# Kernel optimization log

Measured on AMD Instinct MI355X. Metric: run time of the kernel, lower is better.

## Reference

```python
import jax, jax.numpy as jnp
import numpy as np

SEQ, D, H, FF = 2048, 1024, 16, 4096
HD = D // H  # head_dim = 64


def setup_inputs() -> dict:
    key = jax.random.key(0)
    ks = jax.random.split(key, 13)
    s = lambda k, shape, fan_in: jax.random.normal(k, shape, jnp.float32) / np.sqrt(fan_in)
    return {
        "x":  jax.random.normal(ks[0], (SEQ, D), jnp.float32),
        # per-head Q/K/V linears, batched over the head axis: [H, D, HD]
        "Wq": s(ks[1], (H, D, HD), D), "bq": jnp.zeros((H, HD), jnp.float32),
        "Wk": s(ks[2], (H, D, HD), D), "bk": jnp.zeros((H, HD), jnp.float32),
        "Wv": s(ks[3], (H, D, HD), D), "bv": jnp.zeros((H, HD), jnp.float32),
        "Wp": s(ks[4], (D, D), D),     "bp": jnp.zeros((D,), jnp.float32),
        "W1": s(ks[5], (D, FF), D),    "b1": jnp.zeros((FF,), jnp.float32),
        "W2": s(ks[6], (FF, D), FF),   "b2": jnp.zeros((D,), jnp.float32),
    }


def reference(x, Wq, bq, Wk, bk, Wv, bv, Wp, bp, W1, b1, W2, b2):
    # Batched per-head projections: [H, S, HD]
    Qx = jnp.einsum("sd,hde->hse", x, Wq) + bq[:, None, :]
    Kx = jnp.einsum("sd,hde->hse", x, Wk) + bk[:, None, :]
    Vx = jnp.einsum("sd,hde->hse", x, Wv) + bv[:, None, :]
    # scores[h,s,t] = Qx[h,s]. Kx[h,t] / sqrt(HD); softmax over t (last dim)
    scores = jnp.einsum("hse,hte->hst", Qx, Kx) / jnp.sqrt(jnp.float32(HD))
    attn = jax.nn.softmax(scores, axis=-1)
    # Faithful to source: head[t,e] = sum_s Vx[s,e] * attn[s,t]  (attn^T @ V)
    heads = jnp.einsum("hse,hst->hte", Vx, attn)  # [H, S, HD]
    # concat heads along feature dim (head-major order) -> [S, D]
    concat = jnp.transpose(heads, (1, 0, 2)).reshape(SEQ, H * HD)
    proj = concat @ Wp + bp
    hidden = jax.nn.relu(proj @ W1 + b1)
    out = hidden @ W2 + b2
    return out
```

## Files before the change

kernel.cpp:

```cpp
#include <hip/hip_runtime.h>
#include <math.h>

constexpr int S_  = 2048;
constexpr int D_  = 1024;
constexpr int H_  = 16;
constexpr int HD_ = 64;
constexpr int FF_ = 4096;

typedef short bf16x8 __attribute__((ext_vector_type(8)));
typedef float f32x4  __attribute__((ext_vector_type(4)));

static __device__ __forceinline__ ushort f2bf(float f) {
    union { __bf16 b; ushort u; } c;
    c.b = (__bf16)f;
    return c.u;
}
static __device__ __forceinline__ float bf2f(ushort u) {
    return __uint_as_float(((unsigned)u) << 16);
}

static __device__ __forceinline__ float exp8(float x) {
    return __builtin_amdgcn_exp2f(x * 0.18033688f);
}

static __device__ __forceinline__ void gload_lds16(const void* g, void* l) {
    __builtin_amdgcn_global_load_lds(
        (const __attribute__((address_space(1))) unsigned int*)g,
        (__attribute__((address_space(3))) unsigned int*)l, 16, 0, 0);
}

static __device__ __forceinline__ void tc_tile(
    const float* __restrict__ in, ushort* __restrict__ out,
    int K, int N, int n0, int k0)
{
    __shared__ float Ts[32][33];
    const int tid = threadIdx.x;
    const int r = tid >> 3, c4 = (tid & 7) * 4;
    float4 v = *(const float4*)(in + (size_t)(k0 + r) * N + n0 + c4);
    Ts[r][c4 + 0] = v.x; Ts[r][c4 + 1] = v.y;
    Ts[r][c4 + 2] = v.z; Ts[r][c4 + 3] = v.w;
    __syncthreads();
    ushort4 o;
    o.x = f2bf(Ts[c4 + 0][r]); o.y = f2bf(Ts[c4 + 1][r]);
    o.z = f2bf(Ts[c4 + 2][r]); o.w = f2bf(Ts[c4 + 3][r]);
    *(ushort4*)(out + (size_t)(n0 + r) * K + k0 + c4) = o;
}

__global__ __launch_bounds__(256) void pack_all(
    const float* __restrict__ x,
    const float* __restrict__ Wq, const float* __restrict__ Wk,
    const float* __restrict__ Wv, const float* __restrict__ Wp,
    const float* __restrict__ W1, const float* __restrict__ W2,
    const float* __restrict__ bq, const float* __restrict__ bk,
    const float* __restrict__ bv,
    ushort* __restrict__ xb, ushort* __restrict__ BTqkv,
    ushort* __restrict__ BTp, ushort* __restrict__ BT1,
    ushort* __restrict__ BT2, float* __restrict__ biascat)
{
    const int b = blockIdx.x;
    const int tid = threadIdx.x;
    if (b < 2048) {
        const int i = b * 1024 + tid * 4;
        float4 v = *(const float4*)(x + i);
        ushort4 o;
        o.x = f2bf(v.x); o.y = f2bf(v.y); o.z = f2bf(v.z); o.w = f2bf(v.w);
        *(ushort4*)(xb + i) = o;
    } else if (b < 5120) {
        int j = b - 2048;
        const int which = j >> 10;
        j &= 1023;
        const int hh = j >> 6, t = j & 63;
        const float* W = (which == 0) ? Wq : (which == 1) ? Wk : Wv;
        tc_tile(W + hh * 65536, BTqkv + which * 1024 * 1024 + hh * 65536,
                1024, 64, (t & 1) * 32, (t >> 1) * 32);
    } else if (b < 6144) {
        const int j = b - 5120;
        tc_tile(Wp, BTp, 1024, 1024, (j & 31) * 32, (j >> 5) * 32);
    } else if (b < 10240) {
        const int j = b - 6144;
        tc_tile(W1, BT1, 1024, 4096, (j & 127) * 32, (j >> 7) * 32);
    } else if (b < 14336) {
        const int j = b - 10240;
        tc_tile(W2, BT2, 4096, 1024, (j & 31) * 32, (j >> 5) * 32);
    } else {
        const int i = (b - 14336) * 256 + tid;
        float v = (i < 1024) ? bq[i] : (i < 2048 ? bk[i - 1024] : bv[i - 2048]);
        biascat[i] = v;
    }
}

template <int BM, int BN, int WR, int WC, int KS, int RELU, int OUT>
__global__ __launch_bounds__(WR * WC * 64) void gemm_mfma(
    const ushort* __restrict__ A, const ushort* __restrict__ BT,
    const float* __restrict__ bias, void* __restrict__ Cv,
    void* __restrict__ Cv2, int M, int N, int K)
{
    constexpr int WAVES = WR * WC;
    constexpr int WTM = BM / WR, WTN = BN / WC;
    constexpr int MT = WTM / 16, NT = WTN / 16;
    constexpr int AI = BM / 8;
    constexpr int TI = (BM + BN) / 8;
    constexpr int PW = TI / WAVES;

    __shared__ ushort As[BM * 64];
    __shared__ ushort Bs[BN * 64];

    const int tid = threadIdx.x;
    const int lane = tid & 63;
    const int wave = tid >> 6;
    const int wr = wave / WC, wc = wave % WC;
    const int row16 = lane & 15, kgrp = lane >> 4;
    const int m0 = blockIdx.y * BM, n0 = blockIdx.x * BN;
    const int kOff = (KS > 1) ? blockIdx.z * (K / KS) : 0;

    const int lrow = lane >> 3;
    const int sc8 = (lane & 7) ^ lrow;

    f32x4 acc[MT][NT];
#pragma unroll
    for (int i = 0; i < MT; ++i)
#pragma unroll
        for (int j = 0; j < NT; ++j) acc[i][j] = (f32x4){0.f, 0.f, 0.f, 0.f};

    for (int k0 = kOff; k0 < kOff + K / KS; k0 += 64) {
        __syncthreads();
#pragma unroll
        for (int i = 0; i < PW; ++i) {
            const int inst = wave * PW + i;
            if (inst < AI) {
                const int row = inst * 8;
                gload_lds16(A + (size_t)(m0 + row + lrow) * K + k0 + sc8 * 8,
                            As + row * 64);
            } else {
                const int row = (inst - AI) * 8;
                gload_lds16(BT + (size_t)(n0 + row + lrow) * K + k0 + sc8 * 8,
                            Bs + row * 64);
            }
        }
        __syncthreads();
#pragma unroll
        for (int ks = 0; ks < 2; ++ks) {
            bf16x8 af[MT], bfr[NT];
#pragma unroll
            for (int mt = 0; mt < MT; ++mt) {
                const int r = wr * WTM + mt * 16 + row16;
                af[mt] = *(const bf16x8*)(As + r * 64 + (((ks * 4 + kgrp) ^ (r & 7)) * 8));
            }
#pragma unroll
            for (int nt = 0; nt < NT; ++nt) {
                const int r = wc * WTN + nt * 16 + row16;
                bfr[nt] = *(const bf16x8*)(Bs + r * 64 + (((ks * 4 + kgrp) ^ (r & 7)) * 8));
            }
#pragma unroll
            for (int mt = 0; mt < MT; ++mt)
#pragma unroll
                for (int nt = 0; nt < NT; ++nt)
                    acc[mt][nt] = __builtin_amdgcn_mfma_f32_16x16x32_bf16(
                        af[mt], bfr[nt], acc[mt][nt], 0, 0, 0);
        }
    }

    if constexpr (OUT == 2) {
        float* Cp = ((blockIdx.z < KS / 2) ? (float*)Cv : (float*)Cv2)
                    + (size_t)(blockIdx.z % (KS / 2)) * M * N;
#pragma unroll
        for (int nt = 0; nt < NT; ++nt) {
            const int n = n0 + wc * WTN + nt * 16 + row16;
#pragma unroll
            for (int mt = 0; mt < MT; ++mt)
#pragma unroll
                for (int r = 0; r < 4; ++r) {
                    const int m = m0 + wr * WTM + mt * 16 + kgrp * 4 + r;
                    Cp[(size_t)m * N + n] = acc[mt][nt][r];
                }
        }
    } else if constexpr (OUT == 3) {
        ushort* QKo = (ushort*)Cv;
        ushort* VTo = (ushort*)Cv2;
        if (n0 < 2048) {
#pragma unroll
            for (int nt = 0; nt < NT; ++nt) {
                const int n = n0 + wc * WTN + nt * 16 + row16;
                const float bb = bias[n];
#pragma unroll
                for (int mt = 0; mt < MT; ++mt)
#pragma unroll
                    for (int r = 0; r < 4; ++r) {
                        const int m = m0 + wr * WTM + mt * 16 + kgrp * 4 + r;
                        QKo[(size_t)m * 2048 + n] = f2bf(acc[mt][nt][r] + bb);
                    }
            }
        } else {
#pragma unroll
            for (int nt = 0; nt < NT; ++nt) {
                const int n = n0 + wc * WTN + nt * 16 + row16;
                const float bb = bias[n];
#pragma unroll
                for (int mt = 0; mt < MT; ++mt) {
                    const int mb = m0 + wr * WTM + mt * 16 + kgrp * 4;
                    ushort4 o;
                    o.x = f2bf(acc[mt][nt][0] + bb);
                    o.y = f2bf(acc[mt][nt][1] + bb);
                    o.z = f2bf(acc[mt][nt][2] + bb);
                    o.w = f2bf(acc[mt][nt][3] + bb);
                    *(ushort4*)(VTo + (size_t)(n - 2048) * 2048 + mb) = o;
                }
            }
        }
    } else {
#pragma unroll
        for (int nt = 0; nt < NT; ++nt) {
            const int n = n0 + wc * WTN + nt * 16 + row16;
            const float bb = bias ? bias[n] : 0.f;
#pragma unroll
            for (int mt = 0; mt < MT; ++mt)
#pragma unroll
                for (int r = 0; r < 4; ++r) {
                    const int m = m0 + wr * WTM + mt * 16 + kgrp * 4 + r;
                    float v = acc[mt][nt][r] + bb;
                    if (RELU) v = fmaxf(v, 0.f);
                    if (OUT == 1)
                        ((ushort*)Cv)[(size_t)m * N + n] = f2bf(v);
                    else
                        ((float*)Cv)[(size_t)m * N + n] = v;
                }
        }
    }
}

__global__ __launch_bounds__(256) void reduce4_bias(
    const float* __restrict__ pA, const float* __restrict__ pB,
    const float* __restrict__ bias, float* __restrict__ out, int MN, int N)
{
    const int i = (blockIdx.x * 256 + threadIdx.x) * 4;
    float4 a = *(const float4*)(pA + i);
    const float4 b = *(const float4*)(pA + (size_t)MN + i);
    const float4 c = *(const float4*)(pB + i);
    const float4 d = *(const float4*)(pB + (size_t)MN + i);
    const float4 e = *(const float4*)(bias + (i & (N - 1)));
    a.x += b.x + c.x + d.x + e.x;
    a.y += b.y + c.y + d.y + e.y;
    a.z += b.z + c.z + d.z + e.z;
    a.w += b.w + c.w + d.w + e.w;
    *(float4*)(out + i) = a;
}

__global__ __launch_bounds__(256) void reduce2_bias_bf16(
    const float* __restrict__ pA, const float* __restrict__ pB,
    const float* __restrict__ bias, ushort* __restrict__ out, int N)
{
    const int i = (blockIdx.x * 256 + threadIdx.x) * 4;
    const float4 a = *(const float4*)(pA + i);
    const float4 b = *(const float4*)(pB + i);
    const float4 e = *(const float4*)(bias + (i & (N - 1)));
    ushort4 o;
    o.x = f2bf(a.x + b.x + e.x);
    o.y = f2bf(a.y + b.y + e.y);
    o.z = f2bf(a.z + b.z + e.z);
    o.w = f2bf(a.w + b.w + e.w);
    *(ushort4*)(out + i) = o;
}

__global__ __launch_bounds__(256) void attn_stats(
    const ushort* __restrict__ QK, float* __restrict__ part)
{
    const int h = blockIdx.y;
    const int s0 = blockIdx.x * 128;
    const int tz = blockIdx.z;
    const int tid = threadIdx.x;
    const int lane = tid & 63;
    const int w = tid >> 6;
    const int row16 = lane & 15;
    const int kgrp = lane >> 4;

    __shared__ ushort Ks[2][64 * 64];

    bf16x8 qf[2][2];
#pragma unroll
    for (int mt = 0; mt < 2; ++mt) {
        const ushort* qp = QK + (size_t)(s0 + w * 32 + mt * 16 + row16) * 2048 + h * 64;
        qf[mt][0] = *(const bf16x8*)(qp + kgrp * 8);
        qf[mt][1] = *(const bf16x8*)(qp + kgrp * 8 + 32);
    }

    float suml[2][4] = {{0.f}};
    const int lr = lane >> 3;
    const int sw8 = ((lane & 7) ^ lr) * 8;

#pragma unroll
    for (int i = 0; i < 2; ++i) {
        const int inst = w * 2 + i;
        gload_lds16(QK + (size_t)(tz * 512 + inst * 8 + lr) * 2048 + 1024 + h * 64 + sw8,
                    Ks[0] + inst * 512);
    }

    for (int ti = 0; ti < 8; ++ti) {
        __syncthreads();
        if (ti < 7) {
            const int t1 = tz * 512 + (ti + 1) * 64;
            ushort* kb = Ks[(ti + 1) & 1];
#pragma unroll
            for (int i = 0; i < 2; ++i) {
                const int inst = w * 2 + i;
                gload_lds16(QK + (size_t)(t1 + inst * 8 + lr) * 2048 + 1024 + h * 64 + sw8,
                            kb + inst * 512);
            }
        }
        const ushort* Kb = Ks[ti & 1];
#pragma unroll
        for (int nt = 0; nt < 4; ++nt) {
            const int kr = nt * 16 + row16;
            bf16x8 kf0 = *(const bf16x8*)(Kb + kr * 64 + ((kgrp ^ (kr & 7)) * 8));
            bf16x8 kf1 = *(const bf16x8*)(Kb + kr * 64 + (((kgrp + 4) ^ (kr & 7)) * 8));
#pragma unroll
            for (int mt = 0; mt < 2; ++mt) {
                f32x4 sc = (f32x4){0.f, 0.f, 0.f, 0.f};
                sc = __builtin_amdgcn_mfma_f32_16x16x32_bf16(qf[mt][0], kf0, sc, 0, 0, 0);
                sc = __builtin_amdgcn_mfma_f32_16x16x32_bf16(qf[mt][1], kf1, sc, 0, 0, 0);
#pragma unroll
                for (int r = 0; r < 4; ++r)
                    suml[mt][r] += exp8(sc[r]);
            }
        }
    }
#pragma unroll
    for (int mt = 0; mt < 2; ++mt)
#pragma unroll
        for (int r = 0; r < 4; ++r) {
#pragma unroll
            for (int m = 1; m < 16; m <<= 1)
                suml[mt][r] += __shfl_xor(suml[mt][r], m, 64);
        }
    if (row16 == 0) {
#pragma unroll
        for (int mt = 0; mt < 2; ++mt)
#pragma unroll
            for (int r = 0; r < 4; ++r)
                part[((size_t)tz * H_ + h) * S_ + s0 + w * 32 + mt * 16 + kgrp * 4 + r]
                    = suml[mt][r];
    }
}

__global__ __launch_bounds__(256) void attn_pv(
    const ushort* __restrict__ QK, const ushort* __restrict__ VT,
    const float* __restrict__ statsP, ushort* __restrict__ pvp)
{
    const int h = blockIdx.y;
    const int t0 = blockIdx.x * 128;
    const int sbase = blockIdx.z * 512;
    const int tid = threadIdx.x;
    const int lane = tid & 63;
    const int w = tid >> 6;
    const int row16 = lane & 15;
    const int kgrp = lane >> 4;

    __shared__ ushort KP[128 * 64];
    __shared__ ushort Qs[2][64 * 64];
    __shared__ ushort Vs[2][64 * 64];
    __shared__ float  ilL[512];

    const int lr = lane >> 3;
    const int sw8 = ((lane & 7) ^ lr) * 8;

#pragma unroll
    for (int i = 0; i < 4; ++i) {
        const int inst = w * 4 + i;
        gload_lds16(QK + (size_t)(t0 + inst * 8 + lr) * 2048 + 1024 + h * 64 + sw8,
                    KP + inst * 512);
    }
#pragma unroll
    for (int i = 0; i < 2; ++i) {
        const int inst = w * 2 + i;
        const int r = inst * 8 + lr;
        gload_lds16(QK + (size_t)(sbase + r) * 2048 + h * 64 + sw8, Qs[0] + inst * 512);
        gload_lds16(VT + (size_t)(h * 64 + r) * 2048 + sbase + sw8, Vs[0] + inst * 512);
    }
    {
        const int HS = H_ * S_;
#pragma unroll
        for (int k = 0; k < 2; ++k) {
            const int sl = tid * 2 + k;
            const int idx = h * S_ + sbase + sl;
            float s = statsP[idx] + statsP[HS + idx] +
                      statsP[2 * HS + idx] + statsP[3 * HS + idx];
            ilL[sl] = 1.f / s;
        }
    }
    __syncthreads();

    bf16x8 kf[2][2];
#pragma unroll
    for (int nt = 0; nt < 2; ++nt) {
        const int r = w * 32 + nt * 16 + row16;
        kf[nt][0] = *(const bf16x8*)(KP + r * 64 + ((kgrp ^ (r & 7)) * 8));
        kf[nt][1] = *(const bf16x8*)(KP + r * 64 + (((kgrp + 4) ^ (r & 7)) * 8));
    }

    f32x4 acc[2][4];
#pragma unroll
    for (int i = 0; i < 2; ++i)
#pragma unroll
        for (int j = 0; j < 4; ++j) acc[i][j] = (f32x4){0.f, 0.f, 0.f, 0.f};

    for (int si = 0; si < 8; ++si) {
        if (si > 0) __syncthreads();
        if (si < 7) {
            const int s1 = sbase + (si + 1) * 64;
            ushort* qb = Qs[(si + 1) & 1];
            ushort* vb = Vs[(si + 1) & 1];
#pragma unroll
            for (int i = 0; i < 2; ++i) {
                const int inst = w * 2 + i;
                const int r = inst * 8 + lr;
                gload_lds16(QK + (size_t)(s1 + r) * 2048 + h * 64 + sw8, qb + inst * 512);
                gload_lds16(VT + (size_t)(h * 64 + r) * 2048 + s1 + sw8, vb + inst * 512);
            }
        }
        const ushort* Qb = Qs[si & 1];
        const ushort* Vb = Vs[si & 1];

#pragma unroll
        for (int mt = 0; mt < 4; ++mt) {
            const int qr = mt * 16 + row16;
            bf16x8 qf0 = *(const bf16x8*)(Qb + qr * 64 + ((kgrp ^ (qr & 7)) * 8));
            bf16x8 qf1 = *(const bf16x8*)(Qb + qr * 64 + (((kgrp + 4) ^ (qr & 7)) * 8));
            f32x4 il4 = *(const f32x4*)(ilL + si * 64 + mt * 16 + kgrp * 4);
#pragma unroll
            for (int nt = 0; nt < 2; ++nt) {
                f32x4 sc = (f32x4){0.f, 0.f, 0.f, 0.f};
                sc = __builtin_amdgcn_mfma_f32_16x16x32_bf16(qf0, kf[nt][0], sc, 0, 0, 0);
                sc = __builtin_amdgcn_mfma_f32_16x16x32_bf16(qf1, kf[nt][1], sc, 0, 0, 0);
                ushort4 o;
                o.x = f2bf(exp8(sc[0]) * il4[0]);
                o.y = f2bf(exp8(sc[1]) * il4[1]);
                o.z = f2bf(exp8(sc[2]) * il4[2]);
                o.w = f2bf(exp8(sc[3]) * il4[3]);
                const int tl = w * 32 + nt * 16 + row16;
                const int chunk = mt * 2 + (kgrp >> 1);
                *(ushort4*)(KP + tl * 64 + ((chunk ^ (tl & 7)) * 8) + (kgrp & 1) * 4) = o;
            }
        }

        bf16x8 vf[4][2];
#pragma unroll
        for (int nt = 0; nt < 4; ++nt) {
            const int vr = nt * 16 + row16;
            vf[nt][0] = *(const bf16x8*)(Vb + vr * 64 + ((kgrp ^ (vr & 7)) * 8));
            vf[nt][1] = *(const bf16x8*)(Vb + vr * 64 + (((kgrp + 4) ^ (vr & 7)) * 8));
        }
#pragma unroll
        for (int mt = 0; mt < 2; ++mt) {
            const int pr = w * 32 + mt * 16 + row16;
            bf16x8 pf0 = *(const bf16x8*)(KP + pr * 64 + ((kgrp ^ (pr & 7)) * 8));
            bf16x8 pf1 = *(const bf16x8*)(KP + pr * 64 + (((kgrp + 4) ^ (pr & 7)) * 8));
#pragma unroll
            for (int nt = 0; nt < 4; ++nt) {
                acc[mt][nt] = __builtin_amdgcn_mfma_f32_16x16x32_bf16(pf0, vf[nt][0], acc[mt][nt], 0, 0, 0);
                acc[mt][nt] = __builtin_amdgcn_mfma_f32_16x16x32_bf16(pf1, vf[nt][1], acc[mt][nt], 0, 0, 0);
            }
        }
    }

    ushort* dst = pvp + (size_t)blockIdx.z * S_ * D_;
#pragma unroll
    for (int mt = 0; mt < 2; ++mt)
#pragma unroll
        for (int nt = 0; nt < 4; ++nt)
#pragma unroll
            for (int r = 0; r < 4; ++r) {
                const int t = t0 + w * 32 + mt * 16 + kgrp * 4 + r;
                const int e = nt * 16 + row16;
                dst[(size_t)t * D_ + h * 64 + e] = f2bf(acc[mt][nt][r]);
            }
}

__global__ __launch_bounds__(256) void reduce_cat(
    const ushort* __restrict__ p, ushort* __restrict__ concat)
{
    const size_t SD = (size_t)S_ * D_;
    const size_t i = ((size_t)blockIdx.x * 256 + threadIdx.x) * 8;
    union { uint4 u; ushort s[8]; } a, b, c, d, o;
    a.u = *(const uint4*)(p + i);
    b.u = *(const uint4*)(p + SD + i);
    c.u = *(const uint4*)(p + 2 * SD + i);
    d.u = *(const uint4*)(p + 3 * SD + i);
#pragma unroll
    for (int j = 0; j < 8; ++j)
        o.s[j] = f2bf(bf2f(a.s[j]) + bf2f(b.s[j]) + bf2f(c.s[j]) + bf2f(d.s[j]));
    *(uint4*)(concat + i) = o.u;
}

extern "C" void kernel_launch(void* const* d_in, const int* in_sizes, int n_in,
                              void* d_out, int out_size, void* d_ws,
                              size_t ws_size, hipStream_t stream)
{
    const float* x  = (const float*)d_in[0];
    const float* Wq = (const float*)d_in[1];
    const float* bq = (const float*)d_in[2];
    const float* Wk = (const float*)d_in[3];
    const float* bk = (const float*)d_in[4];
    const float* Wv = (const float*)d_in[5];
    const float* bv = (const float*)d_in[6];
    const float* Wp = (const float*)d_in[7];
    const float* bp = (const float*)d_in[8];
    const float* W1 = (const float*)d_in[9];
    const float* b1 = (const float*)d_in[10];
    const float* W2 = (const float*)d_in[11];
    const float* b2 = (const float*)d_in[12];
    float* out = (float*)d_out;

    constexpr size_t MB = 1u << 20;
    char* base = (char*)d_ws;
    ushort* BT2    = (ushort*)(base +  0 * MB);
    ushort* BT1    = (ushort*)(base +  8 * MB);
    ushort* BTp    = (ushort*)(base + 16 * MB);
    ushort* xb     = (ushort*)(base + 18 * MB);
    ushort* concat = (ushort*)(base + 18 * MB);
    ushort* BTqkv  = (ushort*)(base + 22 * MB);
    ushort* projb  = (ushort*)(base + 22 * MB);
    ushort* QKcat  = (ushort*)(base + 28 * MB);
    ushort* VTg    = (ushort*)(base + 36 * MB);
    ushort* pvp    = (ushort*)(base + 40 * MB);
    float*  prjA   = (float*) (base + 28 * MB);
    float*  prjB   = (float*) (base + 36 * MB);
    ushort* hidden = (ushort*)(base + 28 * MB);
    float*  ff2a   = (float*) (base + 44 * MB);
    float*  ff2b   = (float*) (base +  8 * MB);
    float*  biascat= (float*) (base + 60 * MB);
    float*  statsP = biascat + 4096;

    pack_all<<<dim3(14348), 256, 0, stream>>>(
        x, Wq, Wk, Wv, Wp, W1, W2, bq, bk, bv,
        xb, BTqkv, BTp, BT1, BT2, biascat);

    gemm_mfma<128, 128, 2, 2, 1, 0, 3>
        <<<dim3(3072 / 128, S_ / 128, 1), 256, 0, stream>>>(
            xb, BTqkv, biascat, QKcat, VTg, S_, 3072, D_);

    attn_stats<<<dim3(S_ / 128, H_, 4), 256, 0, stream>>>(QKcat, statsP);

    attn_pv<<<dim3(S_ / 128, H_, 4), 256, 0, stream>>>(QKcat, VTg, statsP, pvp);

    reduce_cat<<<dim3(S_ * D_ / 2048), 256, 0, stream>>>(pvp, concat);

    gemm_mfma<64, 128, 1, 4, 2, 0, 2>
        <<<dim3(D_ / 128, S_ / 64, 2), 256, 0, stream>>>(
            concat, BTp, nullptr, prjA, prjB, S_, D_, D_);
    reduce2_bias_bf16<<<dim3(S_ * D_ / 1024), 256, 0, stream>>>(
        prjA, prjB, bp, projb, D_);

    gemm_mfma<128, 128, 2, 2, 1, 1, 1>
        <<<dim3(FF_ / 128, S_ / 128, 1), 256, 0, stream>>>(
            projb, BT1, b1, hidden, nullptr, S_, FF_, D_);

    gemm_mfma<128, 128, 2, 2, 4, 0, 2>
        <<<dim3(D_ / 128, S_ / 128, 4), 256, 0, stream>>>(
            hidden, BT2, nullptr, ff2a, ff2b, S_, D_, FF_);

    reduce4_bias<<<dim3(S_ * D_ / 1024), 256, 0, stream>>>(
        ff2a, ff2b, b2, out, S_ * D_, D_);
}
```

Before: 267.8 us.

## Halve attention split factor and drop split-K for projection GEMM

Attention stats and PV kernels now split the key/sequence axis into 2 chunks of 1024 instead of 4 of 512. This halves partial buffers and the reduction traffic in reduce_cat. The projection GEMM no longer uses split-K with a separate reduce-plus-bias kernel. It runs as a single 64x64-tile GEMM that applies bias and writes bf16 directly, removing a launch and fp32 partial traffic. The cost is fewer blocks per attention launch, longer per-block loops, and smaller GEMM tiles with less reuse.

```diff
diff --git a/kernel.cpp b/kernel.cpp
--- a/kernel.cpp
+++ b/kernel.cpp
@@ -245,22 +245,6 @@
     *(float4*)(out + i) = a;
 }
 
-__global__ __launch_bounds__(256) void reduce2_bias_bf16(
-    const float* __restrict__ pA, const float* __restrict__ pB,
-    const float* __restrict__ bias, ushort* __restrict__ out, int N)
-{
-    const int i = (blockIdx.x * 256 + threadIdx.x) * 4;
-    const float4 a = *(const float4*)(pA + i);
-    const float4 b = *(const float4*)(pB + i);
-    const float4 e = *(const float4*)(bias + (i & (N - 1)));
-    ushort4 o;
-    o.x = f2bf(a.x + b.x + e.x);
-    o.y = f2bf(a.y + b.y + e.y);
-    o.z = f2bf(a.z + b.z + e.z);
-    o.w = f2bf(a.w + b.w + e.w);
-    *(ushort4*)(out + i) = o;
-}
-
 __global__ __launch_bounds__(256) void attn_stats(
     const ushort* __restrict__ QK, float* __restrict__ part)
 {
@@ -290,14 +274,14 @@
 #pragma unroll
     for (int i = 0; i < 2; ++i) {
         const int inst = w * 2 + i;
-        gload_lds16(QK + (size_t)(tz * 512 + inst * 8 + lr) * 2048 + 1024 + h * 64 + sw8,
+        gload_lds16(QK + (size_t)(tz * 1024 + inst * 8 + lr) * 2048 + 1024 + h * 64 + sw8,
                     Ks[0] + inst * 512);
     }
 
-    for (int ti = 0; ti < 8; ++ti) {
+    for (int ti = 0; ti < 16; ++ti) {
         __syncthreads();
-        if (ti < 7) {
-            const int t1 = tz * 512 + (ti + 1) * 64;
+        if (ti < 15) {
+            const int t1 = tz * 1024 + (ti + 1) * 64;
             ushort* kb = Ks[(ti + 1) & 1];
 #pragma unroll
             for (int i = 0; i < 2; ++i) {
@@ -347,7 +331,7 @@
 {
     const int h = blockIdx.y;
     const int t0 = blockIdx.x * 128;
-    const int sbase = blockIdx.z * 512;
+    const int sbase = blockIdx.z * 1024;
     const int tid = threadIdx.x;
     const int lane = tid & 63;
     const int w = tid >> 6;
@@ -357,7 +341,7 @@
     __shared__ ushort KP[128 * 64];
     __shared__ ushort Qs[2][64 * 64];
     __shared__ ushort Vs[2][64 * 64];
-    __shared__ float  ilL[512];
+    __shared__ float  ilL[1024];
 
     const int lr = lane >> 3;
     const int sw8 = ((lane & 7) ^ lr) * 8;
@@ -378,12 +362,10 @@
     {
         const int HS = H_ * S_;
 #pragma unroll
-        for (int k = 0; k < 2; ++k) {
-            const int sl = tid * 2 + k;
+        for (int k = 0; k < 4; ++k) {
+            const int sl = tid * 4 + k;
             const int idx = h * S_ + sbase + sl;
-            float s = statsP[idx] + statsP[HS + idx] +
-                      statsP[2 * HS + idx] + statsP[3 * HS + idx];
-            ilL[sl] = 1.f / s;
+            ilL[sl] = 1.f / (statsP[idx] + statsP[HS + idx]);
         }
     }
     __syncthreads();
@@ -402,9 +384,9 @@
 #pragma unroll
         for (int j = 0; j < 4; ++j) acc[i][j] = (f32x4){0.f, 0.f, 0.f, 0.f};
 
-    for (int si = 0; si < 8; ++si) {
+    for (int si = 0; si < 16; ++si) {
         if (si > 0) __syncthreads();
-        if (si < 7) {
+        if (si < 15) {
             const int s1 = sbase + (si + 1) * 64;
             ushort* qb = Qs[(si + 1) & 1];
             ushort* vb = Vs[(si + 1) & 1];
@@ -479,14 +461,12 @@
 {
     const size_t SD = (size_t)S_ * D_;
     const size_t i = ((size_t)blockIdx.x * 256 + threadIdx.x) * 8;
-    union { uint4 u; ushort s[8]; } a, b, c, d, o;
+    union { uint4 u; ushort s[8]; } a, b, o;
     a.u = *(const uint4*)(p + i);
     b.u = *(const uint4*)(p + SD + i);
-    c.u = *(const uint4*)(p + 2 * SD + i);
-    d.u = *(const uint4*)(p + 3 * SD + i);
 #pragma unroll
     for (int j = 0; j < 8; ++j)
-        o.s[j] = f2bf(bf2f(a.s[j]) + bf2f(b.s[j]) + bf2f(c.s[j]) + bf2f(d.s[j]));
+        o.s[j] = f2bf(bf2f(a.s[j]) + bf2f(b.s[j]));
     *(uint4*)(concat + i) = o.u;
 }
 
@@ -521,8 +501,6 @@
     ushort* QKcat  = (ushort*)(base + 28 * MB);
     ushort* VTg    = (ushort*)(base + 36 * MB);
     ushort* pvp    = (ushort*)(base + 40 * MB);
-    float*  prjA   = (float*) (base + 28 * MB);
-    float*  prjB   = (float*) (base + 36 * MB);
     ushort* hidden = (ushort*)(base + 28 * MB);
     float*  ff2a   = (float*) (base + 44 * MB);
     float*  ff2b   = (float*) (base +  8 * MB);
@@ -537,17 +515,15 @@
         <<<dim3(3072 / 128, S_ / 128, 1), 256, 0, stream>>>(
             xb, BTqkv, biascat, QKcat, VTg, S_, 3072, D_);
 
-    attn_stats<<<dim3(S_ / 128, H_, 4), 256, 0, stream>>>(QKcat, statsP);
-
-    attn_pv<<<dim3(S_ / 128, H_, 4), 256, 0, stream>>>(QKcat, VTg, statsP, pvp);
+    attn_stats<<<dim3(S_ / 128, H_, 2), 256, 0, stream>>>(QKcat, statsP);
+
+    attn_pv<<<dim3(S_ / 128, H_, 2), 256, 0, stream>>>(QKcat, VTg, statsP, pvp);
 
     reduce_cat<<<dim3(S_ * D_ / 2048), 256, 0, stream>>>(pvp, concat);
 
-    gemm_mfma<64, 128, 1, 4, 2, 0, 2>
-        <<<dim3(D_ / 128, S_ / 64, 2), 256, 0, stream>>>(
-            concat, BTp, nullptr, prjA, prjB, S_, D_, D_);
-    reduce2_bias_bf16<<<dim3(S_ * D_ / 1024), 256, 0, stream>>>(
-        prjA, prjB, bp, projb, D_);
+    gemm_mfma<64, 64, 2, 2, 1, 0, 1>
+        <<<dim3(D_ / 64, S_ / 64, 1), 256, 0, stream>>>(
+            concat, BTp, bp, projb, nullptr, S_, D_, D_);
 
     gemm_mfma<128, 128, 2, 2, 1, 1, 1>
         <<<dim3(FF_ / 128, S_ / 128, 1), 256, 0, stream>>>(
```

Measured after the change: 262.8 us. Within noise of the previous version (-1.9%).
